# Optimization experiments

Hardware: AMD Instinct MI355X
Metric: run time of the kernel (lower is better)

## Reference

```python
import jax, jax.numpy as jnp
import numpy as np

B, T, I, C, O = 256, 1024, 128, 256, 10


def setup_inputs() -> dict:
    key = jax.random.key(0)
    k1, k2, k3, k4, k5 = jax.random.split(key, 5)
    x = jax.random.normal(k1, (B, T, I), dtype=jnp.float32)
    # xavier-like scale for kernels
    kernel = jax.random.normal(k2, (I, 2 * C), dtype=jnp.float32) * (6.0 / (I + 2 * C)) ** 0.5
    recurrent_kernel = jax.random.normal(k3, (C, 2 * C), dtype=jnp.float32) * (6.0 / (C + 2 * C)) ** 0.5
    # bias: forget-gate half initialized to log(uniform(1, T-1)), rest zero
    u = jax.random.uniform(k4, (C,), minval=1.0, maxval=float(T - 1))
    recurrent_bias = jnp.concatenate([jnp.log(u), jnp.zeros((C,), jnp.float32)])
    dense_w = jax.random.normal(k5, (C, O), dtype=jnp.float32) * (1.0 / C) ** 0.5
    dense_b = jnp.zeros((O,), jnp.float32)
    return {"x": x, "kernel": kernel, "recurrent_kernel": recurrent_kernel,
            "recurrent_bias": recurrent_bias, "dense_w": dense_w, "dense_b": dense_b}


def reference(x, kernel, recurrent_kernel, recurrent_bias, dense_w, dense_b):
    cells = recurrent_kernel.shape[0]
    # Precompute input projection for all timesteps in one big GEMM: [B,T,2C]
    xz = jnp.einsum('bti,ig->btg', x, kernel) + recurrent_bias
    xz_t = jnp.swapaxes(xz, 0, 1)  # [T, B, 2C] for scan over time

    def step(carry, z_in):
        h, c = carry
        z = z_in + h @ recurrent_kernel  # [B, 2C]
        f = jax.nn.sigmoid(z[:, :cells])
        c_new = f * c + (1.0 - f) * jnp.tanh(z[:, cells:])
        return (c_new, c_new), None

    h0 = jnp.zeros((x.shape[0], cells), x.dtype)
    (h_final, _), _ = jax.lax.scan(step, (h0, h0), xz_t)
    return h_final @ dense_w + dense_b
```

## Files before the change

### kernel.cpp

```cpp
#include <hip/hip_runtime.h>

#define BB 256
#define TT 1024
#define II 128
#define GG 512
#define CC 256
#define L2E 1.44269504f

typedef _Float16 f16;
typedef _Float16 h8_t __attribute__((ext_vector_type(8)));
typedef float f4_t __attribute__((ext_vector_type(4)));
typedef unsigned short ushort_t;
typedef unsigned short us4_t __attribute__((ext_vector_type(4)));

static __device__ __forceinline__ float fast_rcp(float x) {
#if __has_builtin(__builtin_amdgcn_rcpf)
    return __builtin_amdgcn_rcpf(x);
#else
    return 1.f / x;
#endif
}
static __device__ __forceinline__ float fast_exp2(float x) {
#if __has_builtin(__builtin_amdgcn_exp2f)
    return __builtin_amdgcn_exp2f(x);
#else
    return exp2f(x);
#endif
}

__global__ void kt_transpose(const float* __restrict__ kin, f16* __restrict__ kt) {
    int idx = blockIdx.x * 256 + threadIdx.x;
    int k = idx >> 9;
    int n = idx & 511;
    kt[n * II + k] = (f16)kin[k * GG + n];
}

__global__ __launch_bounds__(256)
void gemm_xz(const float* __restrict__ x, const f16* __restrict__ kt,
             const float* __restrict__ bias, ushort_t* __restrict__ xz) {
    const int  ntile = blockIdx.x;
    const long mtile = blockIdx.y;
    const int wave = threadIdx.x >> 6;
    const int lane = threadIdx.x & 63;
    const int wm = (wave & 1) * 64;
    const int wn = (wave >> 1) * 64;
    const int lm = lane & 15;
    const int q  = lane >> 4;

    f4_t acc[4][4];
#pragma unroll
    for (int mi = 0; mi < 4; ++mi)
#pragma unroll
        for (int ni = 0; ni < 4; ++ni)
            acc[mi][ni] = (f4_t){0.f, 0.f, 0.f, 0.f};

#pragma unroll
    for (int kc = 0; kc < 4; ++kc) {
        h8_t a[4], bf[4];
#pragma unroll
        for (int mi = 0; mi < 4; ++mi) {
            const int rowm = (int)(mtile * 128) + wm + mi * 16 + lm;
            const int b  = rowm & 255;
            const int tt = rowm >> 8;
            const float* ap = x + (size_t)b * (TT * II) + (size_t)tt * II + kc * 32 + q * 8;
            f4_t p0 = *(const f4_t*)ap;
            f4_t p1 = *(const f4_t*)(ap + 4);
            h8_t tv;
            tv[0] = (f16)p0[0]; tv[1] = (f16)p0[1]; tv[2] = (f16)p0[2]; tv[3] = (f16)p0[3];
            tv[4] = (f16)p1[0]; tv[5] = (f16)p1[1]; tv[6] = (f16)p1[2]; tv[7] = (f16)p1[3];
            a[mi] = tv;
        }
#pragma unroll
        for (int ni = 0; ni < 4; ++ni) {
            const f16* bp = kt + (size_t)(ntile * 128 + wn + ni * 16 + lm) * II + kc * 32 + q * 8;
            bf[ni] = *(const h8_t*)bp;
        }
#pragma unroll
        for (int mi = 0; mi < 4; ++mi)
#pragma unroll
            for (int ni = 0; ni < 4; ++ni)
                acc[mi][ni] = __builtin_amdgcn_mfma_f32_16x16x32_f16(a[mi], bf[ni], acc[mi][ni], 0, 0, 0);
    }

#pragma unroll
    for (int mi = 0; mi < 4; ++mi) {
        const int rowm0 = (int)(mtile * 128) + wm + mi * 16 + q * 4;
        const int t  = rowm0 >> 8;
        const int b0 = rowm0 & 255;
        const int gq = b0 >> 4;
#pragma unroll
        for (int ni = 0; ni < 4; ++ni) {
            const int col = ntile * 128 + wn + ni * 16 + lm;
            const float bv = bias[col];
            const float s  = (col < CC) ? L2E : (2.0f * L2E);
            us4_t v;
#pragma unroll
            for (int r = 0; r < 4; ++r) {
                f16 hv = (f16)((acc[mi][ni][r] + bv) * s);
                v[r] = *(ushort_t*)&hv;
            }
            *(us4_t*)(xz + (((size_t)t * 16 + gq) * 512 + col) * 16 + q * 4) = v;
        }
    }
}

#define STEP(T, PF, PP, HRD, HWR) do {                                               \
    h8_t af[8];                                                                      \
    _Pragma("unroll") for (int kt = 0; kt < 8; ++kt)                                 \
        af[kt] = *(const h8_t*)((HRD) + lm * 264 + kt * 32 + q * 8);                 \
    f4_t acc[4];                                                                     \
    _Pragma("unroll") for (int ni = 0; ni < 4; ++ni) {                               \
        f4_t av;                                                                     \
        _Pragma("unroll") for (int r = 0; r < 4; ++r) {                              \
            ushort_t u = (PF)[ni * 4 + r];                                           \
            f16 hv = *(f16*)&u;                                                      \
            av[r] = (float)hv;                                                       \
        }                                                                            \
        acc[ni] = av;                                                                \
    }                                                                                \
    if ((T) + 2 < TT) {                                                              \
        _Pragma("unroll") for (int ni = 0; ni < 4; ++ni) {                           \
            us4_t v = *(const us4_t*)((PP) + ni * 2048);                             \
            (PF)[ni * 4 + 0] = v[0];                                                 \
            (PF)[ni * 4 + 1] = v[1];                                                 \
            (PF)[ni * 4 + 2] = v[2];                                                 \
            (PF)[ni * 4 + 3] = v[3];                                                 \
        }                                                                            \
        (PP) += 2 * 131072;                                                          \
    }                                                                                \
                                 \
    _Pragma("unroll") for (int kt = 0; kt < 8; ++kt) {                               \
        acc[0] = __builtin_amdgcn_mfma_f32_16x16x32_f16(af[kt], bw[0][kt], acc[0], 0, 0, 0); \
        acc[2] = __builtin_amdgcn_mfma_f32_16x16x32_f16(af[kt], bw[2][kt], acc[2], 0, 0, 0); \
    }                                                                                \
                                                              \
    _Pragma("unroll") for (int kt = 0; kt < 8; ++kt) {                               \
        acc[1] = __builtin_amdgcn_mfma_f32_16x16x32_f16(af[kt], bw[1][kt], acc[1], 0, 0, 0); \
        acc[3] = __builtin_amdgcn_mfma_f32_16x16x32_f16(af[kt], bw[3][kt], acc[3], 0, 0, 0); \
    }                                                                                \
                       \
    _Pragma("unroll") for (int r = 0; r < 4; ++r) {                                  \
        float zf = acc[0][r];                                                        \
        float zg = acc[2][r];                                                        \
        float ef = fast_exp2(-zf);                                                   \
        float eg = fast_exp2(-fabsf(zg));                                            \
        float t1 = (zg < 0.f) ? -ef : ef;                                            \
        float cv = cst[0][r];                                                        \
        float num = fmaf(cv, eg, cv) + fmaf(-t1, eg, t1);                            \
        float den = (1.f + ef) * (1.f + eg);                                         \
        cst[0][r] = num * fast_rcp(den);                                             \
        (HWR)[(q * 4 + r) * 264 + wave * 16 + lm] = (f16)cst[0][r];                  \
    }                                                                                \
                                                    \
    _Pragma("unroll") for (int r = 0; r < 4; ++r) {                                  \
        float zf = acc[1][r];                                                        \
        float zg = acc[3][r];                                                        \
        float ef = fast_exp2(-zf);                                                   \
        float eg = fast_exp2(-fabsf(zg));                                            \
        float t1 = (zg < 0.f) ? -ef : ef;                                            \
        float cv = cst[1][r];                                                        \
        float num = fmaf(cv, eg, cv) + fmaf(-t1, eg, t1);                            \
        float den = (1.f + ef) * (1.f + eg);                                         \
        cst[1][r] = num * fast_rcp(den);                                             \
        (HWR)[(q * 4 + r) * 264 + (wave + 8) * 16 + lm] = (f16)cst[1][r];            \
    }                                                                                \
    asm volatile("s_waitcnt lgkmcnt(0)\n\ts_barrier" ::: "memory");                  \
} while (0)

__global__ __launch_bounds__(512, 2)
void janet_rec(const float* __restrict__ rk, const float* __restrict__ dw,
               const float* __restrict__ db, const ushort_t* __restrict__ xz,
               float* __restrict__ out) {
    const int g = blockIdx.x;
    const int tid = threadIdx.x;
    const int wave = tid >> 6;
    const int lane = tid & 63;
    const int lm = lane & 15;
    const int q  = lane >> 4;

    h8_t bw[4][8];
#pragma unroll
    for (int ni = 0; ni < 4; ++ni) {
        const float s = (ni < 2) ? L2E : (2.0f * L2E);
#pragma unroll
        for (int kt = 0; kt < 8; ++kt) {
            h8_t tv;
#pragma unroll
            for (int j = 0; j < 8; ++j)
                tv[j] = (f16)(s * rk[(size_t)(kt * 32 + q * 8 + j) * GG + (wave + 8 * ni) * 16 + lm]);
            bw[ni][kt] = tv;
        }
    }

    __shared__ __align__(16) f16 hb[2][16][264];
    f16* h0 = &hb[0][0][0];
    f16* h1 = &hb[1][0][0];
    for (int i = tid; i < 2 * 16 * 264; i += 512) ((f16*)hb)[i] = (f16)0.f;

    float cst[2][4];
#pragma unroll
    for (int ni = 0; ni < 2; ++ni)
#pragma unroll
        for (int r = 0; r < 4; ++r) cst[ni][r] = 0.f;

    const ushort_t* PB = xz + (size_t)g * 8192 + (wave * 16 + lm) * 16 + q * 4;
    const ushort_t* p0 = PB + 2 * 131072;
    const ushort_t* p1 = PB + 3 * 131072;

    ushort_t pf0[16], pf1[16];
#pragma unroll
    for (int ni = 0; ni < 4; ++ni) {
        us4_t v0 = *(const us4_t*)(PB + ni * 2048);
        us4_t v1 = *(const us4_t*)(PB + 131072 + ni * 2048);
        pf0[ni * 4 + 0] = v0[0]; pf0[ni * 4 + 1] = v0[1];
        pf0[ni * 4 + 2] = v0[2]; pf0[ni * 4 + 3] = v0[3];
        pf1[ni * 4 + 0] = v1[0]; pf1[ni * 4 + 1] = v1[1];
        pf1[ni * 4 + 2] = v1[2]; pf1[ni * 4 + 3] = v1[3];
    }
    __syncthreads();

#pragma unroll 1
    for (int t = 0; t < TT; t += 2) {
        STEP(t,     pf0, p0, h0, h1);
        STEP(t + 1, pf1, p1, h1, h0);
    }

    __shared__ float hf[16][256];
#pragma unroll
    for (int ni = 0; ni < 2; ++ni)
#pragma unroll
        for (int r = 0; r < 4; ++r)
            hf[q * 4 + r][(wave + 8 * ni) * 16 + lm] = cst[ni][r];
    __syncthreads();
    if (tid < 160) {
        const int bi = tid / 10, o = tid % 10;
        float acc = db[o];
#pragma unroll 8
        for (int cc = 0; cc < CC; ++cc) acc = fmaf(hf[bi][cc], dw[cc * 10 + o], acc);
        out[(g * 16 + bi) * 10 + o] = acc;
    }
}

__global__ void ws_too_small(float* out, float wssz) {
    int i = blockIdx.x * 256 + threadIdx.x;
    if (i < BB * 10) out[i] = (i == 0) ? wssz : 0.f;
}

extern "C" void kernel_launch(void* const* d_in, const int* in_sizes, int n_in,
                              void* d_out, int out_size, void* d_ws, size_t ws_size,
                              hipStream_t stream) {
    const float* x   = (const float*)d_in[0];
    const float* kin = (const float*)d_in[1];
    const float* rk  = (const float*)d_in[2];
    const float* rb  = (const float*)d_in[3];
    const float* dw  = (const float*)d_in[4];
    const float* db  = (const float*)d_in[5];
    float* out = (float*)d_out;

    const size_t xz_bytes = (size_t)BB * TT * GG * 2;
    const size_t kt_bytes = (size_t)GG * II * 2;
    if (ws_size < xz_bytes + kt_bytes) {
        ws_too_small<<<10, 256, 0, stream>>>(out, (float)ws_size);
        return;
    }

    ushort_t* xz = (ushort_t*)d_ws;
    f16* kt = (f16*)((char*)d_ws + xz_bytes);

    kt_transpose<<<256, 256, 0, stream>>>(kin, kt);
    gemm_xz<<<dim3(4, 2048), 256, 0, stream>>>(x, kt, rb, xz);
    janet_rec<<<16, 512, 0, stream>>>(rk, dw, db, xz, out);
}
```

Baseline: 1.557 ms.

## Split recurrent step barrier into halves and widen GEMM tile to full N

The recurrent step now loads and multiplies the first half of the hidden-state K range, then syncs. It then does the second half, and places a barrier between writing the two halves of the new state. This drops the end-of-step barrier, so the next step can start on columns that are already published while the other half is still being computed. Separately, the input-projection GEMM now uses 512-thread blocks that each cover all 512 output columns, so each x tile is read and converted once instead of four times. The cost is more accumulator registers per wave and a more delicate barrier ordering that relies on the double-buffered state layout.

```diff
diff --git a/kernel.cpp b/kernel.cpp
--- a/kernel.cpp
+++ b/kernel.cpp
@@ -35,28 +35,27 @@
     kt[n * II + k] = (f16)kin[k * GG + n];
 }
 
-__global__ __launch_bounds__(256)
+__global__ __launch_bounds__(512, 2)
 void gemm_xz(const float* __restrict__ x, const f16* __restrict__ kt,
              const float* __restrict__ bias, ushort_t* __restrict__ xz) {
-    const int  ntile = blockIdx.x;
-    const long mtile = blockIdx.y;
+    const long mtile = blockIdx.x;
     const int wave = threadIdx.x >> 6;
     const int lane = threadIdx.x & 63;
     const int wm = (wave & 1) * 64;
-    const int wn = (wave >> 1) * 64;
+    const int wn = (wave >> 1) * 128;
     const int lm = lane & 15;
     const int q  = lane >> 4;
 
-    f4_t acc[4][4];
+    f4_t acc[4][8];
 #pragma unroll
     for (int mi = 0; mi < 4; ++mi)
 #pragma unroll
-        for (int ni = 0; ni < 4; ++ni)
-            acc[mi][ni] = (f4_t){0.f, 0.f, 0.f, 0.f};
+        for (int nj = 0; nj < 8; ++nj)
+            acc[mi][nj] = (f4_t){0.f, 0.f, 0.f, 0.f};
 
 #pragma unroll
     for (int kc = 0; kc < 4; ++kc) {
-        h8_t a[4], bf[4];
+        h8_t a[4], bf[8];
 #pragma unroll
         for (int mi = 0; mi < 4; ++mi) {
             const int rowm = (int)(mtile * 128) + wm + mi * 16 + lm;
@@ -71,15 +70,15 @@
             a[mi] = tv;
         }
 #pragma unroll
-        for (int ni = 0; ni < 4; ++ni) {
-            const f16* bp = kt + (size_t)(ntile * 128 + wn + ni * 16 + lm) * II + kc * 32 + q * 8;
-            bf[ni] = *(const h8_t*)bp;
+        for (int nj = 0; nj < 8; ++nj) {
+            const f16* bp = kt + (size_t)(wn + nj * 16 + lm) * II + kc * 32 + q * 8;
+            bf[nj] = *(const h8_t*)bp;
         }
 #pragma unroll
         for (int mi = 0; mi < 4; ++mi)
 #pragma unroll
-            for (int ni = 0; ni < 4; ++ni)
-                acc[mi][ni] = __builtin_amdgcn_mfma_f32_16x16x32_f16(a[mi], bf[ni], acc[mi][ni], 0, 0, 0);
+            for (int nj = 0; nj < 8; ++nj)
+                acc[mi][nj] = __builtin_amdgcn_mfma_f32_16x16x32_f16(a[mi], bf[nj], acc[mi][nj], 0, 0, 0);
     }
 
 #pragma unroll
@@ -89,14 +88,14 @@
         const int b0 = rowm0 & 255;
         const int gq = b0 >> 4;
 #pragma unroll
-        for (int ni = 0; ni < 4; ++ni) {
-            const int col = ntile * 128 + wn + ni * 16 + lm;
+        for (int nj = 0; nj < 8; ++nj) {
+            const int col = wn + nj * 16 + lm;
             const float bv = bias[col];
             const float s  = (col < CC) ? L2E : (2.0f * L2E);
             us4_t v;
 #pragma unroll
             for (int r = 0; r < 4; ++r) {
-                f16 hv = (f16)((acc[mi][ni][r] + bv) * s);
+                f16 hv = (f16)((acc[mi][nj][r] + bv) * s);
                 v[r] = *(ushort_t*)&hv;
             }
             *(us4_t*)(xz + (((size_t)t * 16 + gq) * 512 + col) * 16 + q * 4) = v;
@@ -106,7 +105,7 @@
 
 #define STEP(T, PF, PP, HRD, HWR) do {                                               \
     h8_t af[8];                                                                      \
-    _Pragma("unroll") for (int kt = 0; kt < 8; ++kt)                                 \
+    _Pragma("unroll") for (int kt = 0; kt < 4; ++kt)                                 \
         af[kt] = *(const h8_t*)((HRD) + lm * 264 + kt * 32 + q * 8);                 \
     f4_t acc[4];                                                                     \
     _Pragma("unroll") for (int ni = 0; ni < 4; ++ni) {                               \
@@ -128,17 +127,28 @@
         }                                                                            \
         (PP) += 2 * 131072;                                                          \
     }                                                                                \
-                                 \
-    _Pragma("unroll") for (int kt = 0; kt < 8; ++kt) {                               \
+                                                  \
+    _Pragma("unroll") for (int kt = 0; kt < 4; ++kt) {                               \
         acc[0] = __builtin_amdgcn_mfma_f32_16x16x32_f16(af[kt], bw[0][kt], acc[0], 0, 0, 0); \
         acc[2] = __builtin_amdgcn_mfma_f32_16x16x32_f16(af[kt], bw[2][kt], acc[2], 0, 0, 0); \
     }                                                                                \
-                                                              \
-    _Pragma("unroll") for (int kt = 0; kt < 8; ++kt) {                               \
+    _Pragma("unroll") for (int kt = 0; kt < 4; ++kt) {                               \
         acc[1] = __builtin_amdgcn_mfma_f32_16x16x32_f16(af[kt], bw[1][kt], acc[1], 0, 0, 0); \
         acc[3] = __builtin_amdgcn_mfma_f32_16x16x32_f16(af[kt], bw[3][kt], acc[3], 0, 0, 0); \
     }                                                                                \
-                       \
+    asm volatile("s_waitcnt lgkmcnt(0)\n\ts_barrier" ::: "memory");       \
+    _Pragma("unroll") for (int kt = 4; kt < 8; ++kt)                                 \
+        af[kt] = *(const h8_t*)((HRD) + lm * 264 + kt * 32 + q * 8);                 \
+         \
+    _Pragma("unroll") for (int kt = 4; kt < 8; ++kt) {                               \
+        acc[0] = __builtin_amdgcn_mfma_f32_16x16x32_f16(af[kt], bw[0][kt], acc[0], 0, 0, 0); \
+        acc[2] = __builtin_amdgcn_mfma_f32_16x16x32_f16(af[kt], bw[2][kt], acc[2], 0, 0, 0); \
+    }                                                                                \
+    _Pragma("unroll") for (int kt = 4; kt < 8; ++kt) {                               \
+        acc[1] = __builtin_amdgcn_mfma_f32_16x16x32_f16(af[kt], bw[1][kt], acc[1], 0, 0, 0); \
+        acc[3] = __builtin_amdgcn_mfma_f32_16x16x32_f16(af[kt], bw[3][kt], acc[3], 0, 0, 0); \
+    }                                                                                \
+                                         \
     _Pragma("unroll") for (int r = 0; r < 4; ++r) {                                  \
         float zf = acc[0][r];                                                        \
         float zg = acc[2][r];                                                        \
@@ -151,7 +161,8 @@
         cst[0][r] = num * fast_rcp(den);                                             \
         (HWR)[(q * 4 + r) * 264 + wave * 16 + lm] = (f16)cst[0][r];                  \
     }                                                                                \
-                                                    \
+    asm volatile("s_waitcnt lgkmcnt(0)\n\ts_barrier" ::: "memory");       \
+          \
     _Pragma("unroll") for (int r = 0; r < 4; ++r) {                                  \
         float zf = acc[1][r];                                                        \
         float zg = acc[3][r];                                                        \
@@ -164,7 +175,6 @@
         cst[1][r] = num * fast_rcp(den);                                             \
         (HWR)[(q * 4 + r) * 264 + (wave + 8) * 16 + lm] = (f16)cst[1][r];            \
     }                                                                                \
-    asm volatile("s_waitcnt lgkmcnt(0)\n\ts_barrier" ::: "memory");                  \
 } while (0)
 
 __global__ __launch_bounds__(512, 2)
@@ -268,6 +278,6 @@
     f16* kt = (f16*)((char*)d_ws + xz_bytes);
 
     kt_transpose<<<256, 256, 0, stream>>>(kin, kt);
-    gemm_xz<<<dim3(4, 2048), 256, 0, stream>>>(x, kt, rb, xz);
+    gemm_xz<<<2048, 512, 0, stream>>>(x, kt, rb, xz);
     janet_rec<<<16, 512, 0, stream>>>(rk, dw, db, xz, out);
 }
```

Measured after the change: 1.464 ms. 5.9% less time.
